# Kernel optimization log

Measured on AMD Instinct MI355X. Metric: run time of the kernel, lower is better.

## Reference

```python
import jax, jax.numpy as jnp
import numpy as np

N_NODES = 20000
N_EDGES = 200000
D_MODEL = 128
N_HEADS = 8
N_LAYERS = 2  # num_gnn - 1 concat layers


def setup_inputs() -> dict:
    key = jax.random.key(0)
    ks = jax.random.split(key, 12)
    s = 0.05  # keep activations well-scaled across residual layers
    hd = D_MODEL // N_HEADS  # 16
    return {
        "x": jax.random.normal(ks[0], (N_NODES, D_MODEL), jnp.float32),
        "src": jax.random.randint(ks[1], (N_EDGES,), 0, N_NODES),
        "dst": jax.random.randint(ks[2], (N_EDGES,), 0, N_NODES),
        "Ws": jax.random.normal(ks[3], (N_LAYERS, D_MODEL, D_MODEL), jnp.float32) * s,
        "als": jax.random.normal(ks[4], (N_LAYERS, N_HEADS, hd), jnp.float32) * s,
        "ars": jax.random.normal(ks[5], (N_LAYERS, N_HEADS, hd), jnp.float32) * s,
        "bs": jax.random.normal(ks[6], (N_LAYERS, D_MODEL), jnp.float32) * s,
        "W_last": jax.random.normal(ks[7], (D_MODEL, N_HEADS * D_MODEL), jnp.float32) * s,
        "al_last": jax.random.normal(ks[8], (N_HEADS, D_MODEL), jnp.float32) * s,
        "ar_last": jax.random.normal(ks[9], (N_HEADS, D_MODEL), jnp.float32) * s,
        "b_last": jax.random.normal(ks[10], (N_HEADS * D_MODEL,), jnp.float32) * s,
    }


def gat_conv(h, src, dst, W, al, ar, b, num_nodes):
    """DGL GATConv (eval mode, dropout off): returns (N, H, D) head outputs."""
    H, D = al.shape
    feat = (h @ W).reshape(num_nodes, H, D)          # (N,H,D)
    el = jnp.sum(feat * al[None], axis=-1)           # (N,H) attn on src side
    er = jnp.sum(feat * ar[None], axis=-1)           # (N,H) attn on dst side
    e = jax.nn.leaky_relu(el[src] + er[dst], 0.2)    # (E,H)
    # edge softmax over incoming edges of each dst node, per head
    m = jax.ops.segment_max(e, dst, num_segments=num_nodes)  # (N,H)
    p = jnp.exp(e - m[dst])                          # (E,H)
    z = jax.ops.segment_sum(p, dst, num_segments=num_nodes)  # (N,H)
    a = p / z[dst]                                   # (E,H)
    msg = feat[src] * a[..., None]                   # (E,H,D) weighted messages
    rst = jax.ops.segment_sum(msg, dst, num_segments=num_nodes)  # (N,H,D)
    return rst + b.reshape(1, H, D)


def reference(x, src, dst, Ws, als, ars, bs, W_last, al_last, ar_last, b_last):
    N = x.shape[0]
    h = x
    for i in range(N_LAYERS):
        temp = gat_conv(h, src, dst, Ws[i], als[i], ars[i], bs[i], N)  # (N,H,hd)
        h = h + jax.nn.elu(temp.reshape(N, -1))       # concat heads, ELU, residual
    temp = gat_conv(h, src, dst, W_last, al_last, ar_last, b_last, N)  # (N,H,D)
    h = h + jnp.mean(temp, axis=1)                    # mean over heads, residual
    return h
```

## Files before the change

### kernel.cpp

```cpp
#include <hip/hip_runtime.h>
#include <math.h>

#define N_NODES 20000
#define N_EDGES 200000
#define DM 128
#define NH 8

typedef __attribute__((ext_vector_type(8))) short bf16x8;
typedef __attribute__((ext_vector_type(4))) float f32x4;

__device__ __forceinline__ unsigned short f2b(float f) {
  unsigned int u = __float_as_uint(f);
  unsigned int r = (u + 0x7FFFu + ((u >> 16) & 1u)) >> 16;
  return (unsigned short)r;
}
__device__ __forceinline__ float b2f(unsigned short s) {
  return __uint_as_float(((unsigned int)s) << 16);
}

__global__ void scan_deg(const int* __restrict__ deg, int* __restrict__ off,
                         int* __restrict__ cursor) {
  __shared__ int part[1024];
  const int tid = threadIdx.x;
  const int CHUNK = (N_NODES + 1023) / 1024;
  int base = tid * CHUNK;
  int s = 0;
  for (int i = 0; i < CHUNK; ++i) {
    int idx = base + i;
    if (idx < N_NODES) s += deg[idx];
  }
  part[tid] = s;
  __syncthreads();
  for (int ofs = 1; ofs < 1024; ofs <<= 1) {
    int v = (tid >= ofs) ? part[tid - ofs] : 0;
    __syncthreads();
    part[tid] += v;
    __syncthreads();
  }
  int run = (tid > 0) ? part[tid - 1] : 0;
  for (int i = 0; i < CHUNK; ++i) {
    int idx = base + i;
    if (idx < N_NODES) {
      off[idx] = run;
      cursor[idx] = run;
      run += deg[idx];
    }
  }
  if (tid == 0) off[N_NODES] = part[1023];
}

__global__ void scatter_e(const int* __restrict__ src, const int* __restrict__ dst,
                          int* __restrict__ cursor, int* __restrict__ csr_src) {
  int e = blockIdx.x * blockDim.x + threadIdx.x;
  if (e < N_EDGES) {
    int p = atomicAdd(&cursor[dst[e]], 1);
    csr_src[p] = src[e];
  }
}

__global__ void prep_w(const float* __restrict__ Ws, unsigned short* __restrict__ wsz,
                       const float* __restrict__ W_last, unsigned short* __restrict__ wpsz,
                       const float* __restrict__ al_last, const float* __restrict__ ar_last,
                       const float* __restrict__ b_last, unsigned short* __restrict__ wlrsz,
                       float* __restrict__ mb, int* __restrict__ deg) {
  int i = blockIdx.x * blockDim.x + threadIdx.x;
  if (i < N_NODES) deg[i] = 0;
  if (i < 2 * 16384) {
    int layer = i >> 14;
    int r = i & 16383;
    int j = r & 7, l = (r >> 3) & 63, f = (r >> 9) & 7, ks = r >> 12;
    int k = ks * 32 + ((l >> 4) << 3) + j;
    int n = f * 16 + (l & 15);
    wsz[i] = f2b(Ws[(size_t)layer * 16384 + k * 128 + n]);
  }
  if (i < 131072) {
    int j = i & 7, l = (i >> 3) & 63, f = (i >> 9) & 7, ks = i >> 12;
    int k = ks * 32 + ((l >> 4) << 3) + j;
    int n = f * 16 + (l & 15);
    int h_ = k >> 7, ko = k & 127;
    wpsz[i] = f2b(W_last[(size_t)ko * 1024 + h_ * 128 + n] * 0.125f);
  }
  if (i < 2048) {
    int j = i & 7, l = (i >> 3) & 63, ks = i >> 9;
    int k = ks * 32 + ((l >> 4) << 3) + j;
    int n = l & 15;
    int hh = n & 7;
    const float* av = (n < 8) ? (al_last + hh * 128) : (ar_last + hh * 128);
    float s = 0.f;
    for (int d = 0; d < 128; ++d) s += W_last[(size_t)k * 1024 + hh * 128 + d] * av[d];
    wlrsz[i] = f2b(s);
  }
  if (i < 128) {
    float s = 0.f;
#pragma unroll
    for (int hh = 0; hh < 8; ++hh) s += b_last[hh * 128 + i];
    mb[i] = s * 0.125f;
  }
}

__global__ void prep_x(const float* __restrict__ x, float* __restrict__ h,
                       unsigned short* __restrict__ hb, const int* __restrict__ dst,
                       int* __restrict__ deg) {
  int i = blockIdx.x * blockDim.x + threadIdx.x;
  if (i < N_NODES * DM) {
    float v = x[i];
    h[i] = v;
    hb[i] = f2b(v);
  }
  if (i < N_EDGES) atomicAdd(&deg[dst[i]], 1);
}

template <int K, bool LAST>
__global__ __launch_bounds__(256) void gemm_mfma(
    const unsigned short* __restrict__ A, const unsigned short* __restrict__ Bsz,
    const float* __restrict__ hres, const float* __restrict__ mb,
    unsigned short* __restrict__ Cb, float* __restrict__ Cf,
    const float* __restrict__ al, const float* __restrict__ ar,
    float* __restrict__ elr) {
  const int tid = threadIdx.x;
  const int lane = tid & 63;
  const int wid = tid >> 6;
  const int wrow = wid & 1, wc = wid >> 1;
  const int r0 = blockIdx.x * 32;
  const int arow = r0 + wrow * 16 + (lane & 15);
  const int kg = lane >> 4;

  f32x4 acc[4];
#pragma unroll
  for (int fi = 0; fi < 4; ++fi) acc[fi] = {0.f, 0.f, 0.f, 0.f};

  const bf16x8* Ap = (const bf16x8*)(A + (size_t)arow * K + kg * 8);
  for (int ks = 0; ks < K / 32; ++ks) {
    bf16x8 a = Ap[ks * 4];
#pragma unroll
    for (int fi = 0; fi < 4; ++fi) {
      int f = wc * 4 + fi;
      bf16x8 b = *(const bf16x8*)(Bsz + (((size_t)(ks * 8 + f) * 64 + lane) << 3));
      acc[fi] = __builtin_amdgcn_mfma_f32_16x16x32_bf16(a, b, acc[fi], 0, 0, 0);
    }
  }

  const int rbase = r0 + wrow * 16 + (lane >> 4) * 4;
#pragma unroll
  for (int fi = 0; fi < 4; ++fi) {
    int col = wc * 64 + fi * 16 + (lane & 15);
#pragma unroll
    for (int r = 0; r < 4; ++r) {
      int row = rbase + r;
      float v = acc[fi][r];
      if (LAST)
        Cf[(size_t)row * DM + col] = v + hres[(size_t)row * DM + col] + mb[col];
      else
        Cb[(size_t)row * DM + col] = f2b(v);
    }
  }

  if (!LAST) {
#pragma unroll
    for (int fi = 0; fi < 4; ++fi) {
      int hh = wc * 4 + fi;
      float alv = al[hh * 16 + (lane & 15)];
      float arv = ar[hh * 16 + (lane & 15)];
#pragma unroll
      for (int r = 0; r < 4; ++r) {
        float pl = acc[fi][r] * alv;
        float pr = acc[fi][r] * arv;
#pragma unroll
        for (int msk = 1; msk < 16; msk <<= 1) {
          pl += __shfl_xor(pl, msk, 64);
          pr += __shfl_xor(pr, msk, 64);
        }
        if ((lane & 15) == 0) {
          int row = rbase + r;
          elr[row * 16 + hh] = pl;
          elr[row * 16 + 8 + hh] = pr;
        }
      }
    }
  }
}

__global__ __launch_bounds__(256) void elr_last(const unsigned short* __restrict__ hb,
                                                const unsigned short* __restrict__ wlrsz,
                                                float* __restrict__ elr) {
  const int lane = threadIdx.x & 63;
  const int wid = threadIdx.x >> 6;
  const int r0 = blockIdx.x * 64 + wid * 16;
  const int arow = r0 + (lane & 15);
  const int kg = lane >> 4;
  f32x4 acc = {0.f, 0.f, 0.f, 0.f};
  int arowc = arow < N_NODES ? arow : N_NODES - 1;
  const bf16x8* Ap = (const bf16x8*)(hb + (size_t)arowc * 128 + kg * 8);
#pragma unroll
  for (int ks = 0; ks < 4; ++ks) {
    bf16x8 a = Ap[ks * 4];
    bf16x8 b = *(const bf16x8*)(wlrsz + (((size_t)ks * 64 + lane) << 3));
    acc = __builtin_amdgcn_mfma_f32_16x16x32_bf16(a, b, acc, 0, 0, 0);
  }
  const int col = lane & 15;
  const int rbase = r0 + (lane >> 4) * 4;
#pragma unroll
  for (int r = 0; r < 4; ++r) {
    int row = rbase + r;
    if (row < N_NODES) elr[row * 16 + col] = acc[r];
  }
}

__global__ __launch_bounds__(256) void fused_small(
    const int* __restrict__ off, const int* __restrict__ csr_src,
    const unsigned short* __restrict__ feat, const float* __restrict__ elr,
    const float* __restrict__ bias, float* __restrict__ h, unsigned short* __restrict__ hb) {
  __shared__ float a_lds[4][64];
  __shared__ int s_lds[4][8];
  __shared__ float zi_lds[4][8];
  const int wid = threadIdx.x >> 6;
  const int t = blockIdx.x * 4 + wid;
  const int lane = threadIdx.x & 63;
  const int e_loc = lane >> 3, hh = lane & 7;
  const int hg = lane >> 3;
  const int beg = off[t], end = off[t + 1];
  const float ert = elr[t * 16 + 8 + hh];

  int e = beg + e_loc;
  bool val = e < end;
  int s = val ? csr_src[e] : 0;
  float xl = val ? elr[s * 16 + hh] : 0.f;

  float z = 0.f, acc0 = 0.f, acc1 = 0.f;
  for (int base = beg; base < end; base += 8) {
    float ex = 0.f;
    if (val) {
      float xv = xl + ert;
      xv = xv > 0.f ? xv : 0.2f * xv;
      ex = __expf(xv);
    }
    a_lds[wid][lane] = ex;
    if (hh == 0) s_lds[wid][e_loc] = s;
    __builtin_amdgcn_wave_barrier();
    asm volatile("s_waitcnt lgkmcnt(0)" ::: "memory");
    z += ex;
    int en = base + 8 + e_loc;
    bool valn = en < end;
    int sn = valn ? csr_src[en] : 0;
    float xln = valn ? elr[sn * 16 + hh] : 0.f;
    int n = min(8, end - base);
    for (int e2 = 0; e2 < n; ++e2) {
      int s2 = s_lds[wid][e2];
      float a = a_lds[wid][e2 * 8 + hg];
      unsigned int hv = *(const unsigned int*)&feat[(size_t)s2 * 128 + 2 * lane];
      acc0 += a * b2f((unsigned short)(hv & 0xffffu));
      acc1 += a * b2f((unsigned short)(hv >> 16));
    }
    __builtin_amdgcn_wave_barrier();
    s = sn;
    xl = xln;
    val = valn;
  }
  z += __shfl_xor(z, 8, 64);
  z += __shfl_xor(z, 16, 64);
  z += __shfl_xor(z, 32, 64);
  if (e_loc == 0) zi_lds[wid][hh] = (z > 0.f) ? 1.f / z : 0.f;
  __builtin_amdgcn_wave_barrier();
  asm volatile("s_waitcnt lgkmcnt(0)" ::: "memory");
  float zi = zi_lds[wid][hg];

  float2 bv = *(const float2*)&bias[2 * lane];
  float v0 = acc0 * zi + bv.x;
  float v1 = acc1 * zi + bv.y;
  v0 = v0 > 0.f ? v0 : expm1f(v0);
  v1 = v1 > 0.f ? v1 : expm1f(v1);
  size_t idx = (size_t)t * 128 + 2 * lane;
  float2 hv = *(const float2*)&h[idx];
  float nh0 = hv.x + v0;
  float nh1 = hv.y + v1;
  *(float2*)&h[idx] = make_float2(nh0, nh1);
  *(ushort2*)&hb[idx] = make_ushort2(f2b(nh0), f2b(nh1));
}

__global__ __launch_bounds__(256) void fused_last(
    const int* __restrict__ off, const int* __restrict__ csr_src,
    const unsigned short* __restrict__ hb, const float* __restrict__ elr,
    unsigned short* __restrict__ g) {
  __shared__ float a_lds[4][64];
  __shared__ int s_lds[4][8];
  __shared__ float zi_lds[4][8];
  const int wid = threadIdx.x >> 6;
  const int t = blockIdx.x * 4 + wid;
  const int lane = threadIdx.x & 63;
  const int e_loc = lane >> 3, hh = lane & 7;
  const int beg = off[t], end = off[t + 1];
  const float ert = elr[t * 16 + 8 + hh];

  int e = beg + e_loc;
  bool val = e < end;
  int s = val ? csr_src[e] : 0;
  float xl = val ? elr[s * 16 + hh] : 0.f;

  float z = 0.f;
  float accA[8], accB[8];
#pragma unroll
  for (int k = 0; k < 8; ++k) accA[k] = accB[k] = 0.f;

  for (int base = beg; base < end; base += 8) {
    float ex = 0.f;
    if (val) {
      float xv = xl + ert;
      xv = xv > 0.f ? xv : 0.2f * xv;
      ex = __expf(xv);
    }
    a_lds[wid][lane] = ex;
    if (hh == 0) s_lds[wid][e_loc] = s;
    __builtin_amdgcn_wave_barrier();
    asm volatile("s_waitcnt lgkmcnt(0)" ::: "memory");
    z += ex;
    int en = base + 8 + e_loc;
    bool valn = en < end;
    int sn = valn ? csr_src[en] : 0;
    float xln = valn ? elr[sn * 16 + hh] : 0.f;
    int n = min(8, end - base);
    for (int e2 = 0; e2 < n; ++e2) {
      int s2 = s_lds[wid][e2];
      float4 pa = *(const float4*)&a_lds[wid][e2 * 8];
      float4 pb = *(const float4*)&a_lds[wid][e2 * 8 + 4];
      unsigned int hv = *(const unsigned int*)&hb[(size_t)s2 * 128 + 2 * lane];
      float h0 = b2f((unsigned short)(hv & 0xffffu));
      float h1 = b2f((unsigned short)(hv >> 16));
      accA[0] += pa.x * h0; accB[0] += pa.x * h1;
      accA[1] += pa.y * h0; accB[1] += pa.y * h1;
      accA[2] += pa.z * h0; accB[2] += pa.z * h1;
      accA[3] += pa.w * h0; accB[3] += pa.w * h1;
      accA[4] += pb.x * h0; accB[4] += pb.x * h1;
      accA[5] += pb.y * h0; accB[5] += pb.y * h1;
      accA[6] += pb.z * h0; accB[6] += pb.z * h1;
      accA[7] += pb.w * h0; accB[7] += pb.w * h1;
    }
    __builtin_amdgcn_wave_barrier();
    s = sn;
    xl = xln;
    val = valn;
  }
  z += __shfl_xor(z, 8, 64);
  z += __shfl_xor(z, 16, 64);
  z += __shfl_xor(z, 32, 64);
  if (e_loc == 0) zi_lds[wid][hh] = (z > 0.f) ? 1.f / z : 0.f;
  __builtin_amdgcn_wave_barrier();
  asm volatile("s_waitcnt lgkmcnt(0)" ::: "memory");
  float4 zia = *(const float4*)&zi_lds[wid][0];
  float4 zib = *(const float4*)&zi_lds[wid][4];
  float ziv[8] = {zia.x, zia.y, zia.z, zia.w, zib.x, zib.y, zib.z, zib.w};
#pragma unroll
  for (int h2 = 0; h2 < 8; ++h2) {
    *(ushort2*)&g[(size_t)t * 1024 + h2 * 128 + 2 * lane] =
        make_ushort2(f2b(accA[h2] * ziv[h2]), f2b(accB[h2] * ziv[h2]));
  }
}

extern "C" void kernel_launch(void* const* d_in, const int* in_sizes, int n_in,
                              void* d_out, int out_size, void* d_ws, size_t ws_size,
                              hipStream_t stream) {
  const float* x = (const float*)d_in[0];
  const int* src = (const int*)d_in[1];
  const int* dst = (const int*)d_in[2];
  const float* Ws = (const float*)d_in[3];
  const float* als = (const float*)d_in[4];
  const float* ars = (const float*)d_in[5];
  const float* bs = (const float*)d_in[6];
  const float* W_last = (const float*)d_in[7];
  const float* al_last = (const float*)d_in[8];
  const float* ar_last = (const float*)d_in[9];
  const float* b_last = (const float*)d_in[10];
  float* out = (float*)d_out;

  float* h = (float*)d_ws;
  float* elr = h + 2560000;
  float* mb = elr + 320000;
  unsigned short* hb = (unsigned short*)(mb + 128);
  unsigned short* feat = hb + 2560000;
  unsigned short* g = feat + 2560000;
  unsigned short* wsz = g + 20480000;
  unsigned short* wpsz = wsz + 32768;
  unsigned short* wlrsz = wpsz + 131072;
  int* deg = (int*)(wlrsz + 2048);
  int* off = deg + N_NODES;
  int* cursor = off + N_NODES + 1;
  int* csr_src = cursor + N_NODES;

  const int ND = N_NODES * DM;

  prep_w<<<512, 256, 0, stream>>>(Ws, wsz, W_last, wpsz, al_last, ar_last, b_last, wlrsz,
                                  mb, deg);
  prep_x<<<(ND + 255) / 256, 256, 0, stream>>>(x, h, hb, dst, deg);
  scan_deg<<<1, 1024, 0, stream>>>(deg, off, cursor);
  scatter_e<<<(N_EDGES + 255) / 256, 256, 0, stream>>>(src, dst, cursor, csr_src);

  const int GB = N_NODES / 32;
  const int FB = N_NODES / 4;
  for (int layer = 0; layer < 2; ++layer) {
    gemm_mfma<DM, false><<<GB, 256, 0, stream>>>(hb, wsz + layer * 16384, nullptr, nullptr,
                                                 feat, nullptr, als + layer * NH * 16,
                                                 ars + layer * NH * 16, elr);
    fused_small<<<FB, 256, 0, stream>>>(off, csr_src, feat, elr, bs + layer * DM, h, hb);
  }

  elr_last<<<(N_NODES + 63) / 64, 256, 0, stream>>>(hb, wlrsz, elr);
  fused_last<<<FB, 256, 0, stream>>>(off, csr_src, hb, elr, g);
  gemm_mfma<NH * DM, true><<<GB, 256, 0, stream>>>(g, wpsz, h, mb, nullptr, out, nullptr,
                                                   nullptr, nullptr);
}
```

Baseline: 199.9 us.

## Fuse prep, degree count/scan, CSR scatter, and last-layer attention logits into fewer launches

```diff
diff --git a/kernel.cpp b/kernel.cpp
--- a/kernel.cpp
+++ b/kernel.cpp
@@ -18,53 +18,21 @@
   return __uint_as_float(((unsigned int)s) << 16);
 }
 
-__global__ void scan_deg(const int* __restrict__ deg, int* __restrict__ off,
-                         int* __restrict__ cursor) {
-  __shared__ int part[1024];
-  const int tid = threadIdx.x;
-  const int CHUNK = (N_NODES + 1023) / 1024;
-  int base = tid * CHUNK;
-  int s = 0;
-  for (int i = 0; i < CHUNK; ++i) {
-    int idx = base + i;
-    if (idx < N_NODES) s += deg[idx];
-  }
-  part[tid] = s;
-  __syncthreads();
-  for (int ofs = 1; ofs < 1024; ofs <<= 1) {
-    int v = (tid >= ofs) ? part[tid - ofs] : 0;
-    __syncthreads();
-    part[tid] += v;
-    __syncthreads();
-  }
-  int run = (tid > 0) ? part[tid - 1] : 0;
-  for (int i = 0; i < CHUNK; ++i) {
-    int idx = base + i;
-    if (idx < N_NODES) {
-      off[idx] = run;
-      cursor[idx] = run;
-      run += deg[idx];
-    }
-  }
-  if (tid == 0) off[N_NODES] = part[1023];
-}
-
-__global__ void scatter_e(const int* __restrict__ src, const int* __restrict__ dst,
-                          int* __restrict__ cursor, int* __restrict__ csr_src) {
-  int e = blockIdx.x * blockDim.x + threadIdx.x;
-  if (e < N_EDGES) {
-    int p = atomicAdd(&cursor[dst[e]], 1);
-    csr_src[p] = src[e];
-  }
-}
-
-__global__ void prep_w(const float* __restrict__ Ws, unsigned short* __restrict__ wsz,
-                       const float* __restrict__ W_last, unsigned short* __restrict__ wpsz,
-                       const float* __restrict__ al_last, const float* __restrict__ ar_last,
-                       const float* __restrict__ b_last, unsigned short* __restrict__ wlrsz,
-                       float* __restrict__ mb, int* __restrict__ deg) {
-  int i = blockIdx.x * blockDim.x + threadIdx.x;
+__global__ __launch_bounds__(256) void prep_all(
+    const float* __restrict__ x, float* __restrict__ h, unsigned short* __restrict__ hb,
+    const float* __restrict__ Ws, unsigned short* __restrict__ wsz,
+    const float* __restrict__ W_last, unsigned short* __restrict__ wpsz,
+    const float* __restrict__ al_last, const float* __restrict__ ar_last,
+    const float* __restrict__ b_last, unsigned short* __restrict__ wlrsz,
+    float* __restrict__ mb, int* __restrict__ deg, int* __restrict__ ticket) {
+  int i = blockIdx.x * 256 + threadIdx.x;
+  if (i < (N_NODES * DM) / 4) {
+    float4 v = ((const float4*)x)[i];
+    ((float4*)h)[i] = v;
+    ((ushort4*)hb)[i] = make_ushort4(f2b(v.x), f2b(v.y), f2b(v.z), f2b(v.w));
+  }
   if (i < N_NODES) deg[i] = 0;
+  if (i == 0) *ticket = 0;
   if (i < 2 * 16384) {
     int layer = i >> 14;
     int r = i & 16383;
@@ -98,30 +66,61 @@
   }
 }
 
-__global__ void prep_x(const float* __restrict__ x, float* __restrict__ h,
-                       unsigned short* __restrict__ hb, const int* __restrict__ dst,
-                       int* __restrict__ deg) {
-  int i = blockIdx.x * blockDim.x + threadIdx.x;
-  if (i < N_NODES * DM) {
-    float v = x[i];
-    h[i] = v;
-    hb[i] = f2b(v);
-  }
-  if (i < N_EDGES) atomicAdd(&deg[dst[i]], 1);
+__global__ __launch_bounds__(256) void count_scan(const int* __restrict__ dst,
+                                                  int* __restrict__ deg,
+                                                  int* __restrict__ off,
+                                                  int* __restrict__ cursor,
+                                                  int* __restrict__ ticket) {
+  int e = blockIdx.x * 256 + threadIdx.x;
+  if (e < N_EDGES) atomicAdd(&deg[dst[e]], 1);
+  __threadfence();
+  __syncthreads();
+  __shared__ int lastFlag;
+  if (threadIdx.x == 0) {
+    int t = __hip_atomic_fetch_add(ticket, 1, __ATOMIC_ACQ_REL, __HIP_MEMORY_SCOPE_AGENT);
+    lastFlag = (t == (int)gridDim.x - 1);
+  }
+  __syncthreads();
+  if (!lastFlag) return;
+
+  __shared__ int part[256];
+  const int tid = threadIdx.x;
+  const int NPT = (N_NODES + 255) / 256;
+  int b0 = tid * NPT, b1 = min(N_NODES, b0 + NPT);
+  int s = 0;
+  for (int j = b0; j < b1; ++j)
+    s += __hip_atomic_load(&deg[j], __ATOMIC_RELAXED, __HIP_MEMORY_SCOPE_AGENT);
+  part[tid] = s;
+  __syncthreads();
+  for (int ofs = 1; ofs < 256; ofs <<= 1) {
+    int v = (tid >= ofs) ? part[tid - ofs] : 0;
+    __syncthreads();
+    part[tid] += v;
+    __syncthreads();
+  }
+  int run = (tid > 0) ? part[tid - 1] : 0;
+  for (int j = b0; j < b1; ++j) {
+    int d = __hip_atomic_load(&deg[j], __ATOMIC_RELAXED, __HIP_MEMORY_SCOPE_AGENT);
+    off[j] = run;
+    cursor[j] = run;
+    run += d;
+  }
+  if (tid == 255) off[N_NODES] = part[255];
+  if (tid == 0) __hip_atomic_store(ticket, 0, __ATOMIC_RELAXED, __HIP_MEMORY_SCOPE_AGENT);
 }
 
 template <int K, bool LAST>
-__global__ __launch_bounds__(256) void gemm_mfma(
-    const unsigned short* __restrict__ A, const unsigned short* __restrict__ Bsz,
-    const float* __restrict__ hres, const float* __restrict__ mb,
-    unsigned short* __restrict__ Cb, float* __restrict__ Cf,
-    const float* __restrict__ al, const float* __restrict__ ar,
-    float* __restrict__ elr) {
-  const int tid = threadIdx.x;
-  const int lane = tid & 63;
-  const int wid = tid >> 6;
+__device__ __forceinline__ void dev_gemm(int tile, const unsigned short* __restrict__ A,
+                                         const unsigned short* __restrict__ Bsz,
+                                         const float* __restrict__ hres,
+                                         const float* __restrict__ mbv,
+                                         unsigned short* __restrict__ Cb,
+                                         float* __restrict__ Cf,
+                                         const float* __restrict__ al,
+                                         const float* __restrict__ ar,
+                                         float* __restrict__ elr, int lane, int wid) {
   const int wrow = wid & 1, wc = wid >> 1;
-  const int r0 = blockIdx.x * 32;
+  const int r0 = tile * 32;
   const int arow = r0 + wrow * 16 + (lane & 15);
   const int kg = lane >> 4;
 
@@ -130,6 +129,7 @@
   for (int fi = 0; fi < 4; ++fi) acc[fi] = {0.f, 0.f, 0.f, 0.f};
 
   const bf16x8* Ap = (const bf16x8*)(A + (size_t)arow * K + kg * 8);
+#pragma unroll 4
   for (int ks = 0; ks < K / 32; ++ks) {
     bf16x8 a = Ap[ks * 4];
 #pragma unroll
@@ -149,7 +149,7 @@
       int row = rbase + r;
       float v = acc[fi][r];
       if (LAST)
-        Cf[(size_t)row * DM + col] = v + hres[(size_t)row * DM + col] + mb[col];
+        Cf[(size_t)row * DM + col] = v + hres[(size_t)row * DM + col] + mbv[col];
       else
         Cb[(size_t)row * DM + col] = f2b(v);
     }
@@ -180,39 +180,44 @@
   }
 }
 
-__global__ __launch_bounds__(256) void elr_last(const unsigned short* __restrict__ hb,
-                                                const unsigned short* __restrict__ wlrsz,
-                                                float* __restrict__ elr) {
-  const int lane = threadIdx.x & 63;
-  const int wid = threadIdx.x >> 6;
-  const int r0 = blockIdx.x * 64 + wid * 16;
-  const int arow = r0 + (lane & 15);
-  const int kg = lane >> 4;
-  f32x4 acc = {0.f, 0.f, 0.f, 0.f};
-  int arowc = arow < N_NODES ? arow : N_NODES - 1;
-  const bf16x8* Ap = (const bf16x8*)(hb + (size_t)arowc * 128 + kg * 8);
-#pragma unroll
-  for (int ks = 0; ks < 4; ++ks) {
-    bf16x8 a = Ap[ks * 4];
-    bf16x8 b = *(const bf16x8*)(wlrsz + (((size_t)ks * 64 + lane) << 3));
-    acc = __builtin_amdgcn_mfma_f32_16x16x32_bf16(a, b, acc, 0, 0, 0);
-  }
-  const int col = lane & 15;
-  const int rbase = r0 + (lane >> 4) * 4;
-#pragma unroll
-  for (int r = 0; r < 4; ++r) {
-    int row = rbase + r;
-    if (row < N_NODES) elr[row * 16 + col] = acc[r];
-  }
-}
-
+__global__ __launch_bounds__(256) void gemm0_scatter(
+    const unsigned short* __restrict__ A, const unsigned short* __restrict__ Bsz,
+    unsigned short* __restrict__ Cb, const float* __restrict__ al,
+    const float* __restrict__ ar, float* __restrict__ elr, const int* __restrict__ srcE,
+    const int* __restrict__ dstE, int* __restrict__ cursor, int* __restrict__ csr_src) {
+  const int bid = blockIdx.x;
+  if (bid < N_NODES / 32) {
+    dev_gemm<DM, false>(bid, A, Bsz, nullptr, nullptr, Cb, nullptr, al, ar, elr,
+                        threadIdx.x & 63, threadIdx.x >> 6);
+  } else {
+    int e = (bid - N_NODES / 32) * 256 + threadIdx.x;
+    if (e < N_EDGES) {
+      int pos = atomicAdd(&cursor[dstE[e]], 1);
+      csr_src[pos] = srcE[e];
+    }
+  }
+}
+
+template <int K, bool LAST>
+__global__ __launch_bounds__(256) void gemm_mfma(
+    const unsigned short* __restrict__ A, const unsigned short* __restrict__ Bsz,
+    const float* __restrict__ hres, const float* __restrict__ mbv,
+    unsigned short* __restrict__ Cb, float* __restrict__ Cf,
+    const float* __restrict__ al, const float* __restrict__ ar, float* __restrict__ elr) {
+  dev_gemm<K, LAST>(blockIdx.x, A, Bsz, hres, mbv, Cb, Cf, al, ar, elr, threadIdx.x & 63,
+                    threadIdx.x >> 6);
+}
+
+template <bool ELR>
 __global__ __launch_bounds__(256) void fused_small(
     const int* __restrict__ off, const int* __restrict__ csr_src,
     const unsigned short* __restrict__ feat, const float* __restrict__ elr,
-    const float* __restrict__ bias, float* __restrict__ h, unsigned short* __restrict__ hb) {
+    const float* __restrict__ bias, float* __restrict__ h, unsigned short* __restrict__ hb,
+    const unsigned short* __restrict__ wlrsz, float* __restrict__ elr_out) {
   __shared__ float a_lds[4][64];
   __shared__ int s_lds[4][8];
   __shared__ float zi_lds[4][8];
+  __shared__ __align__(16) unsigned short nh_lds[4][128];
   const int wid = threadIdx.x >> 6;
   const int t = blockIdx.x * 4 + wid;
   const int lane = threadIdx.x & 63;
@@ -274,7 +279,23 @@
   float nh0 = hv.x + v0;
   float nh1 = hv.y + v1;
   *(float2*)&h[idx] = make_float2(nh0, nh1);
-  *(ushort2*)&hb[idx] = make_ushort2(f2b(nh0), f2b(nh1));
+  unsigned short b0 = f2b(nh0), b1 = f2b(nh1);
+  *(ushort2*)&hb[idx] = make_ushort2(b0, b1);
+
+  if (ELR) {
+    *(ushort2*)&nh_lds[wid][2 * lane] = make_ushort2(b0, b1);
+    __builtin_amdgcn_wave_barrier();
+    asm volatile("s_waitcnt lgkmcnt(0)" ::: "memory");
+    const int kg = lane >> 4;
+    f32x4 acc = {0.f, 0.f, 0.f, 0.f};
+#pragma unroll
+    for (int ks = 0; ks < 4; ++ks) {
+      bf16x8 a = *(const bf16x8*)&nh_lds[wid][ks * 32 + kg * 8];
+      bf16x8 b = *(const bf16x8*)(wlrsz + (((size_t)ks * 64 + lane) << 3));
+      acc = __builtin_amdgcn_mfma_f32_16x16x32_bf16(a, b, acc, 0, 0, 0);
+    }
+    if (lane < 16) elr_out[t * 16 + lane] = acc[0];
+  }
 }
 
 __global__ __launch_bounds__(256) void fused_last(
@@ -373,7 +394,8 @@
 
   float* h = (float*)d_ws;
   float* elr = h + 2560000;
-  float* mb = elr + 320000;
+  float* elr2 = elr + 320000;
+  float* mb = elr2 + 320000;
   unsigned short* hb = (unsigned short*)(mb + 128);
   unsigned short* feat = hb + 2560000;
   unsigned short* g = feat + 2560000;
@@ -384,26 +406,24 @@
   int* off = deg + N_NODES;
   int* cursor = off + N_NODES + 1;
   int* csr_src = cursor + N_NODES;
-
-  const int ND = N_NODES * DM;
-
-  prep_w<<<512, 256, 0, stream>>>(Ws, wsz, W_last, wpsz, al_last, ar_last, b_last, wlrsz,
-                                  mb, deg);
-  prep_x<<<(ND + 255) / 256, 256, 0, stream>>>(x, h, hb, dst, deg);
-  scan_deg<<<1, 1024, 0, stream>>>(deg, off, cursor);
-  scatter_e<<<(N_EDGES + 255) / 256, 256, 0, stream>>>(src, dst, cursor, csr_src);
+  int* ticket = csr_src + N_EDGES;
 
   const int GB = N_NODES / 32;
   const int FB = N_NODES / 4;
-  for (int layer = 0; layer < 2; ++layer) {
-    gemm_mfma<DM, false><<<GB, 256, 0, stream>>>(hb, wsz + layer * 16384, nullptr, nullptr,
-                                                 feat, nullptr, als + layer * NH * 16,
-                                                 ars + layer * NH * 16, elr);
-    fused_small<<<FB, 256, 0, stream>>>(off, csr_src, feat, elr, bs + layer * DM, h, hb);
-  }
-
-  elr_last<<<(N_NODES + 63) / 64, 256, 0, stream>>>(hb, wlrsz, elr);
-  fused_last<<<FB, 256, 0, stream>>>(off, csr_src, hb, elr, g);
+  const int EB = (N_EDGES + 255) / 256;
+
+  prep_all<<<(N_NODES * DM / 4 + 255) / 256, 256, 0, stream>>>(
+      x, h, hb, Ws, wsz, W_last, wpsz, al_last, ar_last, b_last, wlrsz, mb, deg, ticket);
+  count_scan<<<EB, 256, 0, stream>>>(dst, deg, off, cursor, ticket);
+  gemm0_scatter<<<GB + EB, 256, 0, stream>>>(hb, wsz, feat, als, ars, elr, src, dst,
+                                             cursor, csr_src);
+  fused_small<false><<<FB, 256, 0, stream>>>(off, csr_src, feat, elr, bs, h, hb, nullptr,
+                                             nullptr);
+  gemm_mfma<DM, false><<<GB, 256, 0, stream>>>(hb, wsz + 16384, nullptr, nullptr, feat,
+                                               nullptr, als + 128, ars + 128, elr);
+  fused_small<true><<<FB, 256, 0, stream>>>(off, csr_src, feat, elr, bs + 128, h, hb,
+                                            wlrsz, elr2);
+  fused_last<<<FB, 256, 0, stream>>>(off, csr_src, hb, elr2, g);
   gemm_mfma<NH * DM, true><<<GB, 256, 0, stream>>>(g, wpsz, h, mb, nullptr, out, nullptr,
                                                    nullptr, nullptr);
 }
```

Result: slower. 255.6 us, median of 2 (+27.9%).
